# Performance work log

Hardware: AMD Instinct MI355X
Metric: run time of the kernel (lower is better)

Reference implementation:

```python
import jax, jax.numpy as jnp
import numpy as np

H = 256   # lstm2 hidden size
D_IN = 512  # lstm2 input size (256 fed-back out + 256 audio)
BN_EPS = 1e-5


def _lstm_cell(x, h, c, Wih, Whh, bih, bhh):
    # torch gate order: i, f, g, o
    z = x @ Wih.T + h @ Whh.T + bih + bhh  # (B, 4H)
    i, f, g, o = jnp.split(z, 4, axis=-1)
    i = jax.nn.sigmoid(i)
    f = jax.nn.sigmoid(f)
    g = jnp.tanh(g)
    o = jax.nn.sigmoid(o)
    c = f * c + i * g
    h = o * jnp.tanh(c)
    return h, c


def setup_inputs() -> dict:
    key = jax.random.key(0)
    ks = jax.random.split(key, 16)
    B, T, L = 256, 512, 16
    s = 0.05
    inp = {
        "rt": jax.random.normal(ks[0], (B, H), jnp.float32),
        "audio": jax.random.normal(ks[1], (B, T, H), jnp.float32),
        "s_rt": jax.random.normal(ks[2], (B, L, H), jnp.float32),
        # lstm2 layer 0
        "W_ih_l0": jax.random.normal(ks[3], (4 * H, D_IN), jnp.float32) * s,
        "W_hh_l0": jax.random.normal(ks[4], (4 * H, H), jnp.float32) * s,
        "b_ih_l0": jax.random.normal(ks[5], (4 * H,), jnp.float32) * s,
        "b_hh_l0": jax.random.normal(ks[6], (4 * H,), jnp.float32) * s,
        # lstm2 layer 1
        "W_ih_l1": jax.random.normal(ks[7], (4 * H, H), jnp.float32) * s,
        "W_hh_l1": jax.random.normal(ks[8], (4 * H, H), jnp.float32) * s,
        "b_ih_l1": jax.random.normal(ks[9], (4 * H,), jnp.float32) * s,
        "b_hh_l1": jax.random.normal(ks[10], (4 * H,), jnp.float32) * s,
        # rt_linear head: Linear(256,128) -> BN(128) -> ReLU -> Linear(128,6)
        "W1": jax.random.normal(ks[11], (128, H), jnp.float32) * s,
        "b1": jax.random.normal(ks[12], (128,), jnp.float32) * s,
        "gamma": jnp.ones((128,), jnp.float32),
        "beta": jnp.zeros((128,), jnp.float32),
        "W2": jax.random.normal(ks[13], (6, 128), jnp.float32) * s,
        "b2": jax.random.normal(ks[14], (6,), jnp.float32) * s,
        "max_len": 0,
    }
    return inp


def reference(rt, audio, s_rt,
              W_ih_l0, W_hh_l0, b_ih_l0, b_hh_l0,
              W_ih_l1, W_hh_l1, b_ih_l1, b_hh_l1,
              W1, b1, gamma, beta, W2, b2, max_len):
    B, T, _ = audio.shape
    prev_out = jnp.mean(s_rt, axis=1)  # (B, 256): torch.mean(s_rt, dim=1)
    h1 = c1 = h2 = c2 = jnp.zeros((B, H), audio.dtype)

    def step(carry, a_t):
        prev_out, h1, c1, h2, c2 = carry
        x = jnp.concatenate([prev_out, a_t], axis=-1)  # (B, 512)
        h1n, c1n = _lstm_cell(x, h1, c1, W_ih_l0, W_hh_l0, b_ih_l0, b_hh_l0)
        h2n, c2n = _lstm_cell(h1n, h2, c2, W_ih_l1, W_hh_l1, b_ih_l1, b_hh_l1)
        return (h2n, h1n, c1n, h2n, c2n), h2n

    audio_tm = jnp.transpose(audio, (1, 0, 2))  # (T, B, 256) time-major
    _, out_tm = jax.lax.scan(step, (prev_out, h1, c1, h2, c2), audio_tm)
    out = jnp.transpose(out_tm, (1, 0, 2)).reshape(-1, H)  # (B*T, 256)

    # rt_linear head, BatchNorm1d in training mode (batch stats)
    y = out @ W1.T + b1  # (B*T, 128)
    mu = jnp.mean(y, axis=0)
    var = jnp.var(y, axis=0)
    y = (y - mu) * jax.lax.rsqrt(var + BN_EPS) * gamma + beta
    y = jax.nn.relu(y)
    y = y @ W2.T + b2  # (B*T, 6)
    return y.reshape(B, T, -1)
```

## Files before the change

kernel.cpp:

```cpp
#include <hip/hip_runtime.h>
#include <stdint.h>

typedef unsigned int u32;
typedef unsigned short u16;
typedef unsigned long long u64;
typedef _Float16 f16;
typedef _Float16 h2_t __attribute__((ext_vector_type(2)));
typedef _Float16 f16x4 __attribute__((ext_vector_type(4)));
typedef _Float16 f16x8 __attribute__((ext_vector_type(8)));
typedef float f32x4 __attribute__((ext_vector_type(4)));
typedef float f32x16 __attribute__((ext_vector_type(16)));
typedef u32 u32x4 __attribute__((ext_vector_type(4)));

#define TT 512
#define NF 128
#define NTOT (256 * TT)

#define OFF_WA0   0u
#define OFF_WA1   1572864u
#define OFF_WAH   2621440u
#define OFF_GSUM  2883584u
#define OFF_GSQ   2884096u
#define OFF_CTR   2884608u
#define OFF_GH1   2886656u
#define OFF_GH2   3017728u
#define OFF_Y     3148800u

__device__ __forceinline__ float sigf(float x) { return 1.0f / (1.0f + __expf(-x)); }
__device__ __forceinline__ float tanh_fast(float x) { return 1.0f - 2.0f / (__expf(2.0f * x) + 1.0f); }

__global__ void prep_kernel(const float* __restrict__ Wih0, const float* __restrict__ Whh0,
                            const float* __restrict__ Wih1, const float* __restrict__ Whh1,
                            const float* __restrict__ W1,
                            f16* __restrict__ WA0, f16* __restrict__ WA1, f16* __restrict__ WAH,
                            float* __restrict__ gz, u32* __restrict__ ctr) {
    int idx = blockIdx.x * 256 + threadIdx.x;
    const int n0 = 786432, n1 = 524288, n2 = 131072;
    if (idx < n0) {
        int u = idx >> 9, r9 = idx & 511;
        int lane = r9 >> 3, j = r9 & 7;
        int ks = u % 6; u /= 6;
        int wv = u & 7, w = u >> 3;
        int lr = lane & 31, h = lane >> 5;
        int r = ((lr >> 3) << 8) + 8 * w + (lr & 7);
        int seg = ks >> 1, sig = ks & 1;
        int c = 256 * seg + 32 * wv + 16 * sig + 8 * h + j;
        float v = (c < 512) ? Wih0[r * 512 + c] : Whh0[r * 256 + (c - 512)];
        WA0[idx] = (f16)v;
    } else if (idx < n0 + n1) {
        int i2 = idx - n0;
        int lane = (i2 >> 3) & 63, j = i2 & 7;
        int ks = (i2 >> 9) & 3, wv = (i2 >> 11) & 7, w = i2 >> 14;
        int lr = lane & 31, h = lane >> 5;
        int r = ((lr >> 3) << 8) + 8 * w + (lr & 7);
        int sig = ks & 1;
        int c = 32 * wv + 16 * sig + 8 * h + j;
        float v = (ks >> 1) ? Whh1[r * 256 + c] : Wih1[r * 256 + c];
        WA1[i2] = (f16)v;
    } else if (idx < n0 + n1 + n2) {
        int i2 = idx - n0 - n1;
        int u = i2 >> 9, r9 = i2 & 511;
        int lane = r9 >> 3, j = r9 & 7;
        int ks = u & 7, w = u >> 3;
        int m = lane & 15, hh = lane >> 4;
        int k = 32 * ks + 8 * hh + j;
        float v = (m < 4) ? W1[(4 * w + m) * 256 + k] : 0.f;
        WAH[i2] = (f16)v;
    } else if (idx < n0 + n1 + n2 + 256) {
        gz[idx - n0 - n1 - n2] = 0.f;
    } else if (idx < n0 + n1 + n2 + 256 + 512) {
        ctr[idx - n0 - n1 - n2 - 256] = 0u;
    }
}

#define MFMA32L(A, BP, C) (C) = __builtin_amdgcn_mfma_f32_32x32x16_f16( \
    __builtin_bit_cast(f16x8, (A)), __builtin_bit_cast(f16x8, *(const uint4*)(BP)), (C), 0, 0, 0)
#define MFMA32R(A, B, C) (C) = __builtin_amdgcn_mfma_f32_32x32x16_f16( \
    __builtin_bit_cast(f16x8, (A)), __builtin_bit_cast(f16x8, (B)), (C), 0, 0, 0)

#define ZZWR(KW, C) do { \
    f32x4 v0_ = {(C)[0], (C)[1], (C)[2], (C)[3]};    *(f32x4*)&zz[KW][n32][4 * h32] = v0_; \
    f32x4 v1_ = {(C)[4], (C)[5], (C)[6], (C)[7]};    *(f32x4*)&zz[KW][n32][8 + 4 * h32] = v1_; \
    f32x4 v2_ = {(C)[8], (C)[9], (C)[10], (C)[11]};  *(f32x4*)&zz[KW][n32][16 + 4 * h32] = v2_; \
    f32x4 v3_ = {(C)[12], (C)[13], (C)[14], (C)[15]}; *(f32x4*)&zz[KW][n32][24 + 4 * h32] = v3_; } while (0)

#define GATHER2(F0, F1, P0, P1) asm volatile( \
    "global_load_dwordx4 %0, %2, off sc0 sc1\n\t" \
    "global_load_dwordx4 %1, %3, off sc0 sc1\n\t" \
    "s_waitcnt vmcnt(0)" \
    : "=&v"(F0), "=&v"(F1) : "v"(P0), "v"(P1) : "memory")

#define PUBX4(PTR, DATA) asm volatile( \
    "global_store_dwordx4 %0, %1, off sc0 sc1" :: "v"(PTR), "v"(DATA) : "memory")

#define HEAD_BODY(TIDX) do { \
    f32x4 C_ = {}; \
    _Pragma("unroll") \
    for (int ks_ = 0; ks_ < 8; ++ks_) \
        C_ = __builtin_amdgcn_mfma_f32_16x16x32_f16( \
            __builtin_bit_cast(f16x8, ah[ks_]), \
            __builtin_bit_cast(f16x8, \
                *(const uint4*)&Xh2[wv * 16 + (lane & 15)][32 * ks_ + 8 * ((lane >> 4) & 3)]), \
            C_, 0, 0, 0); \
    if (lane < 16) { \
        float y0 = C_[0] + b1s[0], y1 = C_[1] + b1s[1]; \
        float y2 = C_[2] + b1s[2], y3 = C_[3] + b1s[3]; \
        ys0 += y0; yq0 += y0 * y0; ys1 += y1; yq1 += y1 * y1; \
        ys2 += y2; yq2 += y2 * y2; ys3 += y3; yq3 += y3 * y3; \
        f16x4 yp; yp[0] = (f16)y0; yp[1] = (f16)y1; yp[2] = (f16)y2; yp[3] = (f16)y3; \
        int b_ = wv * 16 + lane; \
        ((u64*)ybuf)[((size_t)(g * 32 + b_) * 512 + (TIDX)) * 32 + w] = __builtin_bit_cast(u64, yp); \
    } } while (0)

__global__ __launch_bounds__(512) void lstm_group_kernel(
    const float* __restrict__ audio, const float* __restrict__ s_rt,
    const uint4* __restrict__ WA0, const uint4* __restrict__ WA1, const uint4* __restrict__ WAH,
    const float* __restrict__ bih0, const float* __restrict__ bhh0,
    const float* __restrict__ bih1, const float* __restrict__ bhh1,
    const float* __restrict__ b1, u32* __restrict__ ctr,
    u64* __restrict__ gh1u, u64* __restrict__ gh2u,
    f16* __restrict__ ybuf, float* __restrict__ gsum, float* __restrict__ gsq)
{
    __shared__ __align__(16) f16 Xa[32][264];
    __shared__ __align__(16) f16 Xh2[32][264];
    __shared__ float zz[8][32][36];
    __shared__ __align__(16) f16 hst[32][8];
    __shared__ float bc0s[32], bc1s[32], b1s[4];
    __shared__ float pad_[2700];

    const int tid = threadIdx.x;
    const int w = blockIdx.x >> 3;
    const int g = blockIdx.x & 7;
    const int wv = tid >> 6;
    const int lane = tid & 63;
    const int n32 = lane & 31;
    const int h32 = (lane >> 5) & 1;
    const int ct = tid - 256;
    const int cb = ct >> 3, cj = ct & 7;

    if (tid == 0) { volatile float* vp = pad_; vp[0] = 0.f; }

    u32* const ctr1 = ctr + (g * 2 + 0) * 32;
    u32* const ctr2 = ctr + (g * 2 + 1) * 32;
    u64* const src1 = gh1u + (size_t)g * 2048;
    u64* const src2 = gh2u + (size_t)g * 2048;
    const size_t gbase = (size_t)n32 * 64 + 8 * wv + 2 * h32;

    uint4 a0[6], a1[4], ah[8] = {};
    #pragma unroll
    for (int ks = 0; ks < 6; ++ks) a0[ks] = WA0[((w * 8 + wv) * 6 + ks) * 64 + lane];
    #pragma unroll
    for (int ks = 0; ks < 4; ++ks) a1[ks] = WA1[((w * 8 + wv) * 4 + ks) * 64 + lane];
    if (wv < 2) {
        #pragma unroll
        for (int ks = 0; ks < 8; ++ks) ah[ks] = WAH[(w * 8 + ks) * 64 + lane];
    }

    if (tid < 32) {
        int r = ((tid >> 3) << 8) + 8 * w + (tid & 7);
        bc0s[tid] = bih0[r] + bhh0[r];
        bc1s[tid] = bih1[r] + bhh1[r];
    }
    if (tid < 4) b1s[tid] = b1[4 * w + tid];

    for (int it = tid; it < 32 * 256; it += 512) {
        int b = it >> 8, c = it & 255;
        const float* sp = s_rt + ((size_t)(32 * g + b) * 16) * 256 + c;
        float s = 0.f;
        #pragma unroll
        for (int l = 0; l < 16; ++l) s += sp[l * 256];
        Xh2[b][c] = (f16)(s * 0.0625f);
        Xa[b][c] = (f16)audio[((size_t)(32 * g + b) * 512) * 256 + c];
    }
    __syncthreads();

    u32x4 f20 = *(const u32x4*)&Xh2[n32][32 * wv + 8 * h32];
    u32x4 f21 = *(const u32x4*)&Xh2[n32][32 * wv + 16 + 8 * h32];
    u32x4 f10 = {0, 0, 0, 0}, f11 = {0, 0, 0, 0};
    f32x16 aAcc = {};
    MFMA32L(a0[2], &Xa[n32][32 * wv + 8 * h32], aAcc);
    MFMA32L(a0[3], &Xa[n32][32 * wv + 16 + 8 * h32], aAcc);

    float c1 = 0.f, c2 = 0.f;
    float ys0 = 0, ys1 = 0, ys2 = 0, ys3 = 0, yq0 = 0, yq1 = 0, yq2 = 0, yq3 = 0;

    for (int t = 0; t < TT; ++t) {
        const u32 T = (u32)(t + 1);
        MFMA32R(a0[0], f20, aAcc);
        MFMA32R(a0[1], f21, aAcc);
        ZZWR(wv, aAcc);
        __syncthreads();
        if (tid >= 256) {
            float z0 = bc0s[cj], z1 = bc0s[8 + cj], z2 = bc0s[16 + cj], z3 = bc0s[24 + cj];
            #pragma unroll
            for (int kw = 0; kw < 8; ++kw) {
                z0 += zz[kw][cb][cj];      z1 += zz[kw][cb][8 + cj];
                z2 += zz[kw][cb][16 + cj]; z3 += zz[kw][cb][24 + cj];
            }
            float c = sigf(z1) * c1 + sigf(z0) * tanh_fast(z2);
            c1 = c;
            hst[cb][cj] = (f16)(sigf(z3) * tanh_fast(c));
        }
        __syncthreads();
        if (wv == 7 && lane < 32) {
            u32x4 hv = *((const u32x4*)hst + lane);
            PUBX4((void*)(src1 + (size_t)lane * 64 + 2 * w), hv);
        }
        f32x16 Dacc = {};
        if (t > 0) {
            MFMA32R(a1[2], f20, Dacc);
            MFMA32R(a1[3], f21, Dacc);
        }
        if (wv < 2 && t > 0) HEAD_BODY(t - 1);
        if (wv == 7) {
            asm volatile("s_waitcnt vmcnt(0)" ::: "memory");
            if (lane == 0) {
                __hip_atomic_fetch_add(ctr1, 1u, __ATOMIC_RELAXED, __HIP_MEMORY_SCOPE_AGENT);
                u32 tgt = 32u * T; int gu = 0;
                while (__hip_atomic_load(ctr1, __ATOMIC_RELAXED, __HIP_MEMORY_SCOPE_AGENT) < tgt
                       && ++gu < 100000000) { }
            }
        }
        __syncthreads();
        GATHER2(f10, f11, (const void*)(src1 + gbase), (const void*)(src1 + gbase + 4));
        float4 av0, av1, av2, av3;
        if (t + 1 < TT) {
            const float4* a4 = (const float4*)audio;
            int b0 = tid >> 6, q0 = tid & 63;
            size_t base = ((size_t)(t + 1)) * 64 + q0;
            av0 = a4[(size_t)(32 * g + b0) * 32768 + base];
            av1 = a4[(size_t)(32 * g + b0 + 8) * 32768 + base];
            av2 = a4[(size_t)(32 * g + b0 + 16) * 32768 + base];
            av3 = a4[(size_t)(32 * g + b0 + 24) * 32768 + base];
        }
        MFMA32R(a1[0], f10, Dacc);
        MFMA32R(a1[1], f11, Dacc);
        ZZWR(wv, Dacc);
        __syncthreads();
        if (tid >= 256) {
            float z0 = bc1s[cj], z1 = bc1s[8 + cj], z2 = bc1s[16 + cj], z3 = bc1s[24 + cj];
            #pragma unroll
            for (int kw = 0; kw < 8; ++kw) {
                z0 += zz[kw][cb][cj];      z1 += zz[kw][cb][8 + cj];
                z2 += zz[kw][cb][16 + cj]; z3 += zz[kw][cb][24 + cj];
            }
            float c = sigf(z1) * c2 + sigf(z0) * tanh_fast(z2);
            c2 = c;
            hst[cb][cj] = (f16)(sigf(z3) * tanh_fast(c));
        }
        __syncthreads();
        if (wv == 7 && lane < 32) {
            u32x4 hv = *((const u32x4*)hst + lane);
            PUBX4((void*)(src2 + (size_t)lane * 64 + 2 * w), hv);
        }
        if (t + 1 < TT) {
            #define AST(AV, S) do { \
                int b_ = (tid >> 6) + 8 * (S); int q_ = tid & 63; \
                h2_t p0_; p0_.x = (f16)(AV).x; p0_.y = (f16)(AV).y; \
                h2_t p1_; p1_.x = (f16)(AV).z; p1_.y = (f16)(AV).w; \
                uint2 pv_; pv_.x = __builtin_bit_cast(u32, p0_); pv_.y = __builtin_bit_cast(u32, p1_); \
                *(uint2*)&Xa[b_][4 * q_] = pv_; } while (0)
            AST(av0, 0); AST(av1, 1); AST(av2, 2); AST(av3, 3);
        }
        __syncthreads();
        aAcc = (f32x16){};
        if (t + 1 < TT) {
            MFMA32L(a0[2], &Xa[n32][32 * wv + 8 * h32], aAcc);
            MFMA32L(a0[3], &Xa[n32][32 * wv + 16 + 8 * h32], aAcc);
            MFMA32R(a0[4], f10, aAcc);
            MFMA32R(a0[5], f11, aAcc);
        }
        if (wv == 7) {
            asm volatile("s_waitcnt vmcnt(0)" ::: "memory");
            if (lane == 0) {
                __hip_atomic_fetch_add(ctr2, 1u, __ATOMIC_RELAXED, __HIP_MEMORY_SCOPE_AGENT);
                u32 tgt = 32u * T; int gu = 0;
                while (__hip_atomic_load(ctr2, __ATOMIC_RELAXED, __HIP_MEMORY_SCOPE_AGENT) < tgt
                       && ++gu < 100000000) { }
            }
        }
        __syncthreads();
        GATHER2(f20, f21, (const void*)(src2 + gbase), (const void*)(src2 + gbase + 4));
        *(u32x4*)&Xh2[n32][32 * wv + 8 * h32] = f20;
        *(u32x4*)&Xh2[n32][32 * wv + 16 + 8 * h32] = f21;
    }
    __syncthreads();
    if (wv < 2) HEAD_BODY(TT - 1);
    if (wv < 2 && lane < 16) {
        #pragma unroll
        for (int m = 8; m >= 1; m >>= 1) {
            ys0 += __shfl_xor(ys0, m, 64); ys1 += __shfl_xor(ys1, m, 64);
            ys2 += __shfl_xor(ys2, m, 64); ys3 += __shfl_xor(ys3, m, 64);
            yq0 += __shfl_xor(yq0, m, 64); yq1 += __shfl_xor(yq1, m, 64);
            yq2 += __shfl_xor(yq2, m, 64); yq3 += __shfl_xor(yq3, m, 64);
        }
        if (lane == 0) {
            atomicAdd(&gsum[4 * w + 0], ys0); atomicAdd(&gsum[4 * w + 1], ys1);
            atomicAdd(&gsum[4 * w + 2], ys2); atomicAdd(&gsum[4 * w + 3], ys3);
            atomicAdd(&gsq[4 * w + 0], yq0); atomicAdd(&gsq[4 * w + 1], yq1);
            atomicAdd(&gsq[4 * w + 2], yq2); atomicAdd(&gsq[4 * w + 3], yq3);
        }
    }
}

__global__ __launch_bounds__(256) void head_kernel(
    const f16* __restrict__ ybuf, const float* __restrict__ gsum, const float* __restrict__ gsq,
    const float* __restrict__ gamma, const float* __restrict__ beta,
    const float* __restrict__ W2, const float* __restrict__ b2,
    float* __restrict__ out)
{
    __shared__ float sc[NF], sh[NF], W2s[6 * NF], b2s[6];
    const int tid = threadIdx.x;
    if (tid < NF) {
        const float invN = 1.f / (float)NTOT;
        float mu = gsum[tid] * invN;
        float var = gsq[tid] * invN - mu * mu;
        float iv = rsqrtf(var + 1e-5f);
        float s = gamma[tid] * iv;
        sc[tid] = s;
        sh[tid] = beta[tid] - mu * s;
    }
    for (int i = tid; i < 6 * NF; i += 256) W2s[i] = W2[i];
    if (tid < 6) b2s[tid] = b2[tid];
    __syncthreads();

    size_t n = (size_t)blockIdx.x * 256 + tid;
    const h2_t* yr = (const h2_t*)(ybuf + n * NF);
    float a0 = b2s[0], a1 = b2s[1], a2 = b2s[2], a3 = b2s[3], a4 = b2s[4], a5 = b2s[5];
    #pragma unroll 8
    for (int p = 0; p < 64; ++p) {
        h2_t v = yr[p];
        int f0 = 2 * p, f1 = 2 * p + 1;
        float v0 = fmaxf(fmaf((float)v.x, sc[f0], sh[f0]), 0.f);
        float v1 = fmaxf(fmaf((float)v.y, sc[f1], sh[f1]), 0.f);
        a0 = fmaf(v0, W2s[0 * NF + f0], a0); a0 = fmaf(v1, W2s[0 * NF + f1], a0);
        a1 = fmaf(v0, W2s[1 * NF + f0], a1); a1 = fmaf(v1, W2s[1 * NF + f1], a1);
        a2 = fmaf(v0, W2s[2 * NF + f0], a2); a2 = fmaf(v1, W2s[2 * NF + f1], a2);
        a3 = fmaf(v0, W2s[3 * NF + f0], a3); a3 = fmaf(v1, W2s[3 * NF + f1], a3);
        a4 = fmaf(v0, W2s[4 * NF + f0], a4); a4 = fmaf(v1, W2s[4 * NF + f1], a4);
        a5 = fmaf(v0, W2s[5 * NF + f0], a5); a5 = fmaf(v1, W2s[5 * NF + f1], a5);
    }
    float* op = out + n * 6;
    op[0] = a0; op[1] = a1; op[2] = a2; op[3] = a3; op[4] = a4; op[5] = a5;
}

extern "C" void kernel_launch(void* const* d_in, const int* in_sizes, int n_in,
                              void* d_out, int out_size, void* d_ws, size_t ws_size,
                              hipStream_t stream) {
    const float* audio = (const float*)d_in[1];
    const float* s_rt  = (const float*)d_in[2];
    const float* Wih0  = (const float*)d_in[3];
    const float* Whh0  = (const float*)d_in[4];
    const float* bih0  = (const float*)d_in[5];
    const float* bhh0  = (const float*)d_in[6];
    const float* Wih1  = (const float*)d_in[7];
    const float* Whh1  = (const float*)d_in[8];
    const float* bih1  = (const float*)d_in[9];
    const float* bhh1  = (const float*)d_in[10];
    const float* W1    = (const float*)d_in[11];
    const float* b1    = (const float*)d_in[12];
    const float* gamma = (const float*)d_in[13];
    const float* beta  = (const float*)d_in[14];
    const float* W2    = (const float*)d_in[15];
    const float* b2    = (const float*)d_in[16];

    char* ws = (char*)d_ws;
    f16* WA0    = (f16*)(ws + OFF_WA0);
    f16* WA1    = (f16*)(ws + OFF_WA1);
    f16* WAH    = (f16*)(ws + OFF_WAH);
    float* gsum = (float*)(ws + OFF_GSUM);
    float* gsq  = (float*)(ws + OFF_GSQ);
    u32* ctrp   = (u32*)(ws + OFF_CTR);
    u64* gh1u   = (u64*)(ws + OFF_GH1);
    u64* gh2u   = (u64*)(ws + OFF_GH2);
    f16* ybuf   = (f16*)(ws + OFF_Y);
    float* out  = (float*)d_out;

    prep_kernel<<<5635, 256, 0, stream>>>(Wih0, Whh0, Wih1, Whh1, W1,
                                          WA0, WA1, WAH, gsum, ctrp);

    lstm_group_kernel<<<256, 512, 0, stream>>>(audio, s_rt,
                                               (const uint4*)WA0, (const uint4*)WA1, (const uint4*)WAH,
                                               bih0, bhh0, bih1, bhh1, b1, ctrp,
                                               gh1u, gh2u, ybuf, gsum, gsq);

    head_kernel<<<NTOT / 256, 256, 0, stream>>>(ybuf, gsum, gsq, gamma, beta, W2, b2, out);
}
```

Before: 3.314 ms.

## Publish hidden state directly from cell threads and drop per-step block barriers

Cell-update waves now pack h via lane shuffles and store it to global memory themselves, removing the hst staging buffer and its barriers. Each of the four cell waves increments the group counter, and every wave polls the counter directly instead of waiting on a single-lane spin followed by a __syncthreads. Audio prefetch moves one step further ahead, so the shared-memory store of audio happens earlier. Together these remove several __syncthreads per timestep. The trade-offs are much more global polling traffic and a poll cap lowered to 300000 iterations, which could let a wave read stale data on a long stall.

```diff
diff --git a/kernel.cpp b/kernel.cpp
--- a/kernel.cpp
+++ b/kernel.cpp
@@ -93,6 +93,11 @@
 #define PUBX4(PTR, DATA) asm volatile( \
     "global_store_dwordx4 %0, %1, off sc0 sc1" :: "v"(PTR), "v"(DATA) : "memory")
 
+#define POLL(CTRP, TGT) do { \
+    int gu_ = 0; \
+    while (__hip_atomic_load((CTRP), __ATOMIC_RELAXED, __HIP_MEMORY_SCOPE_AGENT) < (TGT) \
+           && ++gu_ < 300000) {} } while (0)
+
 #define HEAD_BODY(TIDX) do { \
     f32x4 C_ = {}; \
     _Pragma("unroll") \
@@ -112,6 +117,32 @@
         ((u64*)ybuf)[((size_t)(g * 32 + b_) * 512 + (TIDX)) * 32 + w] = __builtin_bit_cast(u64, yp); \
     } } while (0)
 
+#define CELL_PUBLISH(BCS, CSTATE, SRC, CTRP) do { \
+    float z0 = BCS[cj], z1 = BCS[8 + cj], z2 = BCS[16 + cj], z3 = BCS[24 + cj]; \
+    _Pragma("unroll") \
+    for (int kw_ = 0; kw_ < 8; ++kw_) { \
+        z0 += zz[kw_][cb][cj];      z1 += zz[kw_][cb][8 + cj]; \
+        z2 += zz[kw_][cb][16 + cj]; z3 += zz[kw_][cb][24 + cj]; \
+    } \
+    float c_ = sigf(z1) * (CSTATE) + sigf(z0) * tanh_fast(z2); \
+    (CSTATE) = c_; \
+    f16 hf_ = (f16)(sigf(z3) * tanh_fast(c_)); \
+    u32 hb_ = (u32)__builtin_bit_cast(u16, hf_); \
+    u32 p01_ = hb_ | ((u32)__shfl_xor((int)hb_, 1, 64) << 16); \
+    u32 p23_ = (u32)__shfl_xor((int)p01_, 2, 64); \
+    u32 p45_ = (u32)__shfl_xor((int)p01_, 4, 64); \
+    u32 p67_ = (u32)__shfl_xor((int)p23_, 4, 64); \
+    if (cj == 0) { \
+        u32x4 word_ = {p01_, p23_, p45_, p67_}; \
+        PUBX4((void*)((SRC) + ((cb << 5) + w) * 2), word_); \
+    } } while (0)
+
+#define DRAIN_COUNT(CTRP) do { \
+    asm volatile("s_waitcnt vmcnt(0)" ::: "memory"); \
+    if ((ct & 63) == 0) \
+        __hip_atomic_fetch_add((CTRP), 1u, __ATOMIC_RELAXED, __HIP_MEMORY_SCOPE_AGENT); \
+    } while (0)
+
 __global__ __launch_bounds__(512) void lstm_group_kernel(
     const float* __restrict__ audio, const float* __restrict__ s_rt,
     const uint4* __restrict__ WA0, const uint4* __restrict__ WA1, const uint4* __restrict__ WAH,
@@ -124,7 +155,6 @@
     __shared__ __align__(16) f16 Xa[32][264];
     __shared__ __align__(16) f16 Xh2[32][264];
     __shared__ float zz[8][32][36];
-    __shared__ __align__(16) f16 hst[32][8];
     __shared__ float bc0s[32], bc1s[32], b1s[4];
     __shared__ float pad_[2700];
 
@@ -137,6 +167,7 @@
     const int h32 = (lane >> 5) & 1;
     const int ct = tid - 256;
     const int cb = ct >> 3, cj = ct & 7;
+    const int ab0 = tid >> 6, aq0 = tid & 63;
 
     if (tid == 0) { volatile float* vp = pad_; vp[0] = 0.f; }
 
@@ -172,6 +203,15 @@
         Xh2[b][c] = (f16)(s * 0.0625f);
         Xa[b][c] = (f16)audio[((size_t)(32 * g + b) * 512) * 256 + c];
     }
+    float4 av0, av1, av2, av3;
+    {
+        const float4* a4 = (const float4*)audio;
+        size_t base = 64 + aq0;
+        av0 = a4[(size_t)(32 * g + ab0) * 32768 + base];
+        av1 = a4[(size_t)(32 * g + ab0 + 8) * 32768 + base];
+        av2 = a4[(size_t)(32 * g + ab0 + 16) * 32768 + base];
+        av3 = a4[(size_t)(32 * g + ab0 + 24) * 32768 + base];
+    }
     __syncthreads();
 
     u32x4 f20 = *(const u32x4*)&Xh2[n32][32 * wv + 8 * h32];
@@ -190,101 +230,64 @@
         MFMA32R(a0[1], f21, aAcc);
         ZZWR(wv, aAcc);
         __syncthreads();
-        if (tid >= 256) {
-            float z0 = bc0s[cj], z1 = bc0s[8 + cj], z2 = bc0s[16 + cj], z3 = bc0s[24 + cj];
-            #pragma unroll
-            for (int kw = 0; kw < 8; ++kw) {
-                z0 += zz[kw][cb][cj];      z1 += zz[kw][cb][8 + cj];
-                z2 += zz[kw][cb][16 + cj]; z3 += zz[kw][cb][24 + cj];
-            }
-            float c = sigf(z1) * c1 + sigf(z0) * tanh_fast(z2);
-            c1 = c;
-            hst[cb][cj] = (f16)(sigf(z3) * tanh_fast(c));
-        }
-        __syncthreads();
-        if (wv == 7 && lane < 32) {
-            u32x4 hv = *((const u32x4*)hst + lane);
-            PUBX4((void*)(src1 + (size_t)lane * 64 + 2 * w), hv);
-        }
+
         f32x16 Dacc = {};
-        if (t > 0) {
-            MFMA32R(a1[2], f20, Dacc);
-            MFMA32R(a1[3], f21, Dacc);
-        }
-        if (wv < 2 && t > 0) HEAD_BODY(t - 1);
-        if (wv == 7) {
-            asm volatile("s_waitcnt vmcnt(0)" ::: "memory");
-            if (lane == 0) {
-                __hip_atomic_fetch_add(ctr1, 1u, __ATOMIC_RELAXED, __HIP_MEMORY_SCOPE_AGENT);
-                u32 tgt = 32u * T; int gu = 0;
-                while (__hip_atomic_load(ctr1, __ATOMIC_RELAXED, __HIP_MEMORY_SCOPE_AGENT) < tgt
-                       && ++gu < 100000000) { }
-            }
-        }
-        __syncthreads();
+        if (wv >= 4) {
+            CELL_PUBLISH(bc0s, c1, src1, ctr1);
+            if (t > 0) { MFMA32R(a1[2], f20, Dacc); MFMA32R(a1[3], f21, Dacc); }
+            DRAIN_COUNT(ctr1);
+        } else {
+            if (t > 0) { MFMA32R(a1[2], f20, Dacc); MFMA32R(a1[3], f21, Dacc); }
+            if (wv < 2 && t > 0) HEAD_BODY(t - 1);
+        }
+        if (t + 1 < TT) {
+            #define AST(AV, S) do { \
+                int b_ = ab0 + 8 * (S); \
+                h2_t p0_; p0_.x = (f16)(AV).x; p0_.y = (f16)(AV).y; \
+                h2_t p1_; p1_.x = (f16)(AV).z; p1_.y = (f16)(AV).w; \
+                uint2 pv_; pv_.x = __builtin_bit_cast(u32, p0_); pv_.y = __builtin_bit_cast(u32, p1_); \
+                *(uint2*)&Xa[b_][4 * aq0] = pv_; } while (0)
+            AST(av0, 0); AST(av1, 1); AST(av2, 2); AST(av3, 3);
+        }
+        POLL(ctr1, 128u * T);
         GATHER2(f10, f11, (const void*)(src1 + gbase), (const void*)(src1 + gbase + 4));
-        float4 av0, av1, av2, av3;
-        if (t + 1 < TT) {
+        if (t + 2 < TT) {
             const float4* a4 = (const float4*)audio;
-            int b0 = tid >> 6, q0 = tid & 63;
-            size_t base = ((size_t)(t + 1)) * 64 + q0;
-            av0 = a4[(size_t)(32 * g + b0) * 32768 + base];
-            av1 = a4[(size_t)(32 * g + b0 + 8) * 32768 + base];
-            av2 = a4[(size_t)(32 * g + b0 + 16) * 32768 + base];
-            av3 = a4[(size_t)(32 * g + b0 + 24) * 32768 + base];
+            size_t base = (size_t)(t + 2) * 64 + aq0;
+            av0 = a4[(size_t)(32 * g + ab0) * 32768 + base];
+            av1 = a4[(size_t)(32 * g + ab0 + 8) * 32768 + base];
+            av2 = a4[(size_t)(32 * g + ab0 + 16) * 32768 + base];
+            av3 = a4[(size_t)(32 * g + ab0 + 24) * 32768 + base];
         }
         MFMA32R(a1[0], f10, Dacc);
         MFMA32R(a1[1], f11, Dacc);
         ZZWR(wv, Dacc);
         __syncthreads();
-        if (tid >= 256) {
-            float z0 = bc1s[cj], z1 = bc1s[8 + cj], z2 = bc1s[16 + cj], z3 = bc1s[24 + cj];
-            #pragma unroll
-            for (int kw = 0; kw < 8; ++kw) {
-                z0 += zz[kw][cb][cj];      z1 += zz[kw][cb][8 + cj];
-                z2 += zz[kw][cb][16 + cj]; z3 += zz[kw][cb][24 + cj];
+
+        aAcc = (f32x16){};
+        if (wv >= 4) {
+            CELL_PUBLISH(bc1s, c2, src2, ctr2);
+            if (t + 1 < TT) {
+                MFMA32L(a0[2], &Xa[n32][32 * wv + 8 * h32], aAcc);
+                MFMA32L(a0[3], &Xa[n32][32 * wv + 16 + 8 * h32], aAcc);
+                MFMA32R(a0[4], f10, aAcc);
+                MFMA32R(a0[5], f11, aAcc);
             }
-            float c = sigf(z1) * c2 + sigf(z0) * tanh_fast(z2);
-            c2 = c;
-            hst[cb][cj] = (f16)(sigf(z3) * tanh_fast(c));
-        }
-        __syncthreads();
-        if (wv == 7 && lane < 32) {
-            u32x4 hv = *((const u32x4*)hst + lane);
-            PUBX4((void*)(src2 + (size_t)lane * 64 + 2 * w), hv);
-        }
-        if (t + 1 < TT) {
-            #define AST(AV, S) do { \
-                int b_ = (tid >> 6) + 8 * (S); int q_ = tid & 63; \
-                h2_t p0_; p0_.x = (f16)(AV).x; p0_.y = (f16)(AV).y; \
-                h2_t p1_; p1_.x = (f16)(AV).z; p1_.y = (f16)(AV).w; \
-                uint2 pv_; pv_.x = __builtin_bit_cast(u32, p0_); pv_.y = __builtin_bit_cast(u32, p1_); \
-                *(uint2*)&Xa[b_][4 * q_] = pv_; } while (0)
-            AST(av0, 0); AST(av1, 1); AST(av2, 2); AST(av3, 3);
-        }
-        __syncthreads();
-        aAcc = (f32x16){};
-        if (t + 1 < TT) {
-            MFMA32L(a0[2], &Xa[n32][32 * wv + 8 * h32], aAcc);
-            MFMA32L(a0[3], &Xa[n32][32 * wv + 16 + 8 * h32], aAcc);
-            MFMA32R(a0[4], f10, aAcc);
-            MFMA32R(a0[5], f11, aAcc);
-        }
-        if (wv == 7) {
-            asm volatile("s_waitcnt vmcnt(0)" ::: "memory");
-            if (lane == 0) {
-                __hip_atomic_fetch_add(ctr2, 1u, __ATOMIC_RELAXED, __HIP_MEMORY_SCOPE_AGENT);
-                u32 tgt = 32u * T; int gu = 0;
-                while (__hip_atomic_load(ctr2, __ATOMIC_RELAXED, __HIP_MEMORY_SCOPE_AGENT) < tgt
-                       && ++gu < 100000000) { }
+            DRAIN_COUNT(ctr2);
+        } else {
+            if (t + 1 < TT) {
+                MFMA32L(a0[2], &Xa[n32][32 * wv + 8 * h32], aAcc);
+                MFMA32L(a0[3], &Xa[n32][32 * wv + 16 + 8 * h32], aAcc);
+                MFMA32R(a0[4], f10, aAcc);
+                MFMA32R(a0[5], f11, aAcc);
             }
         }
-        __syncthreads();
+        POLL(ctr2, 128u * T);
         GATHER2(f20, f21, (const void*)(src2 + gbase), (const void*)(src2 + gbase + 4));
         *(u32x4*)&Xh2[n32][32 * wv + 8 * h32] = f20;
         *(u32x4*)&Xh2[n32][32 * wv + 16 + 8 * h32] = f21;
-    }
-    __syncthreads();
+        __syncthreads();
+    }
     if (wv < 2) HEAD_BODY(TT - 1);
     if (wv < 2 && lane < 16) {
         #pragma unroll
```

Result: slower. 13.24 ms (+299.6%).
